# Kernel tuning notes

Hardware: AMD Instinct MI355X
Metric: run time of the kernel (lower is better)

The kernel has to match this reference:

```python
import jax, jax.numpy as jnp
import numpy as np

B, T, C, K, V = 4, 4096, 128, 64, 64
EPS = 1e-5


def layer_norm(x, g, b):
    mu = jnp.mean(x, axis=-1, keepdims=True)
    var = jnp.var(x, axis=-1, keepdims=True)
    return (x - mu) * jax.lax.rsqrt(var + EPS) * g + b


def setup_inputs() -> dict:
    key = jax.random.key(0)
    ks = jax.random.split(key, 8)
    s = 1.0 / np.sqrt(C)
    return {
        "x": jax.random.normal(ks[0], (B, T, C), dtype=jnp.float32),
        "Wq": jax.random.uniform(ks[1], (C, K), jnp.float32, -s, s),
        "bq": jnp.zeros((K,), jnp.float32),
        "Wk": jax.random.uniform(ks[2], (C, K), jnp.float32, -s, s),
        "bk": jnp.zeros((K,), jnp.float32),
        "Wv": jax.random.uniform(ks[3], (C, V), jnp.float32, -s, s),
        "bv": jnp.zeros((V,), jnp.float32),
        "gq": jnp.ones((K,), jnp.float32), "bgq": jnp.zeros((K,), jnp.float32),
        "gk": jnp.ones((K,), jnp.float32), "bgk": jnp.zeros((K,), jnp.float32),
        "gv": jnp.ones((V,), jnp.float32), "bgv": jnp.zeros((V,), jnp.float32),
        "go": jnp.ones((V,), jnp.float32), "bgo": jnp.zeros((V,), jnp.float32),
    }


def reference(x, Wq, bq, Wk, bk, Wv, bv, gq, bgq, gk, bgk, gv, bgv, go, bgo):
    # projections: B x T x {K,K,V}
    q = layer_norm(x @ Wq + bq, gq, bgq)
    k = layer_norm(x @ Wk + bk, gk, bgk)
    v = layer_norm(x @ Wv + bv, gv, bgv)
    sqrt_k = jnp.asarray(np.sqrt(K), x.dtype)
    # full B x T x T causal score matrix (faithful to the original bmm+mask)
    logits = jnp.einsum("btk,bsk->bts", q, k) / sqrt_k
    t = jnp.arange(T)
    causal = t[:, None] >= t[None, :]  # lower-triangular incl. diagonal
    logits = jnp.where(causal[None], logits, -jnp.inf)
    probs = jax.nn.softmax(logits, axis=-1)
    read = jnp.einsum("bts,bsv->btv", probs, v)
    read = layer_norm(read, go, bgo)
    return jnp.concatenate([x, read], axis=2)  # B x T x (C+V)
```

## Files before the change

### kernel.cpp

```cpp
#include <hip/hip_runtime.h>

#define TT 4096

typedef unsigned short u16;
typedef unsigned int u32;

typedef short bf16x8 __attribute__((ext_vector_type(8)));
typedef float f32x4 __attribute__((ext_vector_type(4)));

union U8 {
  uint2 q[2];
  uint4 u4;
  bf16x8 v;
  short s[8];
  u32 w[4];
};

static __device__ __forceinline__ u16 f2bf(float f) {
  union { float f; u32 u; } cv;
  cv.f = f;
  u32 r = cv.u + 0x7FFFu + ((cv.u >> 16) & 1u);
  return (u16)(r >> 16);
}
static __device__ __forceinline__ u32 pk2(float a, float b) {
  return (u32)f2bf(a) | ((u32)f2bf(b) << 16);
}
static __device__ __forceinline__ float bf2f(u16 h) {
  union { u32 u; float f; } cv;
  cv.u = ((u32)h) << 16;
  return cv.f;
}
static __device__ __forceinline__ float exp2a(float x) {
  float r; asm("v_exp_f32 %0, %1" : "=v"(r) : "v"(x)); return r;
}
static __device__ __forceinline__ u32 cvtpk(float lo, float hi) {
  u32 r; asm("v_cvt_pk_bf16_f32 %0, %1, %2" : "=v"(r) : "v"(lo), "v"(hi)); return r;
}

__global__ __launch_bounds__(64)
void wpack(const float* __restrict__ Wq, const float* __restrict__ Wk,
           const float* __restrict__ Wv, u16* __restrict__ wf)
{
  const int g = blockIdx.x;
  const int p = g >> 4, s = (g >> 2) & 3, nt = g & 3;
  const int l = threadIdx.x, lg = l >> 4, l15 = l & 15;
  const float* W = (p == 0) ? Wq : (p == 1) ? Wk : Wv;
  const int n = l15 + 16 * nt;
  U8 o;
#pragma unroll
  for (int j = 0; j < 8; ++j) {
    int k = 32 * s + ((j < 4) ? (4 * lg + j) : (16 + 4 * lg + (j - 4)));
    o.s[j] = (short)f2bf(W[k * 64 + n]);
  }
  *(uint4*)(wf + (size_t)(g * 64 + l) * 8) = o.u4;
}

__global__ __launch_bounds__(256)
void proj_mfma(const float* __restrict__ x, const u16* __restrict__ wf,
               const float* __restrict__ bq, const float* __restrict__ bk,
               const float* __restrict__ bv,
               const float* __restrict__ gq, const float* __restrict__ bgq,
               const float* __restrict__ gk, const float* __restrict__ bgk,
               const float* __restrict__ gv, const float* __restrict__ bgv,
               u16* __restrict__ qo, u16* __restrict__ ko, u16* __restrict__ vto,
               float* __restrict__ out)
{
  __shared__ u16 xs[64 * 128];
  const int bx = blockIdx.x;
  const int xcd = bx & 7, i = bx >> 3;
  const int tile = xcd * 32 + (i & 31);
  const int p = i >> 5;
  const int rowbase = tile * 64;
  const int t = threadIdx.x;

  {
    const int row = t >> 2, seg = t & 3;
    const float4* src = (const float4*)(x + (size_t)(rowbase + row) * 128 + seg * 32);
    float4 f[8];
#pragma unroll
    for (int q = 0; q < 8; ++q) f[q] = src[q];
    if ((p == 0 && seg < 2) || (p == 1 && seg >= 2)) {
      float4* dst = (float4*)(out + (size_t)(rowbase + row) * 192 + seg * 32);
#pragma unroll
      for (int q = 0; q < 8; ++q) dst[q] = f[q];
    }
    const int base = row * 256 + seg * 64;
    const int swz = (row & 7) << 4;
    char* xb = (char*)xs;
#pragma unroll
    for (int q = 0; q < 4; ++q) {
      uint4 u;
      u.x = pk2(f[2 * q].x, f[2 * q].y);
      u.y = pk2(f[2 * q].z, f[2 * q].w);
      u.z = pk2(f[2 * q + 1].x, f[2 * q + 1].y);
      u.w = pk2(f[2 * q + 1].z, f[2 * q + 1].w);
      *(uint4*)(xb + ((base + 16 * q) ^ swz)) = u;
    }
  }

  const int w = t >> 6, l = t & 63, lg = l >> 4, l15 = l & 15;
  U8 bfr[4][4];
  const u16* wp = wf + (size_t)p * (16 * 64 * 8);
#pragma unroll
  for (int s = 0; s < 4; ++s)
#pragma unroll
    for (int nt = 0; nt < 4; ++nt)
      bfr[s][nt].u4 = *(const uint4*)(wp + ((s * 4 + nt) * 64 + l) * 8);

  __syncthreads();

  f32x4 acc[4];
#pragma unroll
  for (int nt = 0; nt < 4; ++nt) acc[nt] = (f32x4){0.f, 0.f, 0.f, 0.f};
  const int abase = (16 * w + l15) * 256;
  const int aswz = (l15 & 7) << 4;
  const char* xb = (const char*)xs;
#pragma unroll
  for (int s = 0; s < 4; ++s) {
    U8 af;
    af.q[0] = *(const uint2*)(xb + ((abase + s * 64 + 8 * lg) ^ aswz));
    af.q[1] = *(const uint2*)(xb + ((abase + s * 64 + 8 * lg + 32) ^ aswz));
#pragma unroll
    for (int nt = 0; nt < 4; ++nt)
      acc[nt] = __builtin_amdgcn_mfma_f32_16x16x32_bf16(af.v, bfr[s][nt].v, acc[nt], 0, 0, 0);
  }

  const float* bb = (p == 0) ? bq : (p == 1) ? bk : bv;
  const float* gg = (p == 0) ? gq : (p == 1) ? gk : gv;
  const float* hh = (p == 0) ? bgq : (p == 1) ? bgk : bgv;
  float bcol[4], gcol[4], hcol[4];
#pragma unroll
  for (int nt = 0; nt < 4; ++nt) {
    int col = l15 + 16 * nt;
    bcol[nt] = bb[col]; gcol[nt] = gg[col]; hcol[nt] = hh[col];
  }
  float vals[4][4];
#pragma unroll
  for (int nt = 0; nt < 4; ++nt)
#pragma unroll
    for (int r = 0; r < 4; ++r) vals[nt][r] = acc[nt][r] + bcol[nt];

  float s1[4], s2[4];
#pragma unroll
  for (int r = 0; r < 4; ++r) {
    s1[r] = vals[0][r] + vals[1][r] + vals[2][r] + vals[3][r];
    s2[r] = vals[0][r] * vals[0][r] + vals[1][r] * vals[1][r]
          + vals[2][r] * vals[2][r] + vals[3][r] * vals[3][r];
#pragma unroll
    for (int d = 1; d < 16; d <<= 1) {
      s1[r] += __shfl_xor(s1[r], d);
      s2[r] += __shfl_xor(s2[r], d);
    }
  }

  if (p < 2) {
    u16* dst = (p == 0) ? qo : ko;
#pragma unroll
    for (int r = 0; r < 4; ++r) {
      float mu = s1[r] * (1.f / 64.f);
      float var = s2[r] * (1.f / 64.f) - mu * mu;
      float rs = rsqrtf(var + 1e-5f);
      int grow = rowbase + 16 * w + 4 * lg + r;
#pragma unroll
      for (int nt = 0; nt < 4; ++nt)
        dst[(size_t)grow * 64 + l15 + 16 * nt] =
            f2bf((vals[nt][r] - mu) * rs * gcol[nt] + hcol[nt]);
    }
  } else {
    const int b = rowbase >> 12;
    const int tl0 = (rowbase & 4095) + 16 * w + 4 * lg;
#pragma unroll
    for (int r = 0; r < 4; ++r) {
      float mu = s1[r] * (1.f / 64.f);
      float var = s2[r] * (1.f / 64.f) - mu * mu;
      float rs = rsqrtf(var + 1e-5f);
#pragma unroll
      for (int nt = 0; nt < 4; ++nt)
        vto[(size_t)(b * 64 + l15 + 16 * nt) * TT + tl0 + r] =
            f2bf((vals[nt][r] - mu) * rs * gcol[nt] + hcol[nt]);
    }
  }
}

__global__ __launch_bounds__(256)
void attn_seg4(const u16* __restrict__ qg, const u16* __restrict__ kg,
               const u16* __restrict__ vtg,
               float* __restrict__ mP, float* __restrict__ lP,
               u16* __restrict__ aP)
{
  __shared__ u16 kl4[4 * 64 * 64];
  __shared__ u16 vl4[4 * 64 * 64];
  const int bx = blockIdx.x;
  const int xcd = bx & 7, b = xcd >> 1, e = xcd & 1;
  const int j = e * 272 + (bx >> 3);
  int Q = 0;
  while (2 * (Q + 1) * (Q + 2) <= j) ++Q;
  const int ip = j - 2 * Q * (Q + 1);
  const int dv = ip / (Q + 1);
  const int q = 4 * Q + dv;
  const int s = ip - dv * (Q + 1);
  const int q0 = q * 64;
  const int it0 = s * 4;
  const int it1 = min(it0 + 4, q + 1);

  const int t = threadIdx.x;
  const int w = t >> 6, l = t & 63;
  const int l15 = l & 15, lg = l >> 4;
  const int swzl = (l15 & 7) << 4;

  const int qrow = q0 + 16 * w + l15;
  const u16* qrp = qg + (size_t)(b * TT + qrow) * 64;
  U8 qf[2];
#pragma unroll
  for (int hh = 0; hh < 2; ++hh) {
    qf[hh].q[0] = *(const uint2*)(qrp + 32 * hh + 4 * lg);
    qf[hh].q[1] = *(const uint2*)(qrp + 32 * hh + 4 * lg + 16);
  }

  {
    const int key = t >> 2, part = t & 3;
    const int sbase = key * 128 + part * 32;
    const int ssw = (key & 7) << 4;
    uint4 kr[4][2], vr[4][2];
#pragma unroll
    for (int tt = 0; tt < 4; ++tt) {
      int tile = it0 + tt; if (tile >= it1) tile = it1 - 1;
      const u16* ks = kg + (size_t)(b * TT + tile * 64 + key) * 64 + part * 16;
      kr[tt][0] = ((const uint4*)ks)[0];
      kr[tt][1] = ((const uint4*)ks)[1];
      const u16* vs = vtg + (size_t)(b * 64 + key) * TT + tile * 64 + part * 16;
      vr[tt][0] = ((const uint4*)vs)[0];
      vr[tt][1] = ((const uint4*)vs)[1];
    }
#pragma unroll
    for (int tt = 0; tt < 4; ++tt) {
      char* kd = (char*)kl4 + tt * 8192;
      char* vd = (char*)vl4 + tt * 8192;
      *(uint4*)(kd + ((sbase + 0) ^ ssw)) = kr[tt][0];
      *(uint4*)(kd + ((sbase + 16) ^ ssw)) = kr[tt][1];
      *(uint4*)(vd + ((sbase + 0) ^ ssw)) = vr[tt][0];
      *(uint4*)(vd + ((sbase + 16) ^ ssw)) = vr[tt][1];
    }
  }
  __syncthreads();

  const float C = 0.18033688011112042f;
  float m_run = -1e30f, l_run = 0.f;
  f32x4 acc[4];
#pragma unroll
  for (int ct = 0; ct < 4; ++ct) acc[ct] = (f32x4){0.f, 0.f, 0.f, 0.f};

  int toff = 0;
  for (int it = it0; it < it1; ++it, toff += 8192) {
    const int kb = it * 64;
    const char* kp = (const char*)kl4 + toff;
    const char* vp = (const char*)vl4 + toff;

    f32x4 st[4];
    __builtin_amdgcn_s_setprio(1);
#pragma unroll
    for (int t4 = 0; t4 < 4; ++t4) {
      const int rbase = (16 * t4 + l15) * 128 + 8 * lg;
      U8 kf0, kf1;
      kf0.q[0] = *(const uint2*)(kp + ((rbase + 0) ^ swzl));
      kf0.q[1] = *(const uint2*)(kp + ((rbase + 32) ^ swzl));
      kf1.q[0] = *(const uint2*)(kp + ((rbase + 64) ^ swzl));
      kf1.q[1] = *(const uint2*)(kp + ((rbase + 96) ^ swzl));
      f32x4 d = {0.f, 0.f, 0.f, 0.f};
      d = __builtin_amdgcn_mfma_f32_16x16x32_bf16(kf0.v, qf[0].v, d, 0, 0, 0);
      d = __builtin_amdgcn_mfma_f32_16x16x32_bf16(kf1.v, qf[1].v, d, 0, 0, 0);
      st[t4] = d;
    }
    __builtin_amdgcn_s_setprio(0);

    float sv[16];
    const bool needmask = (kb + 63 > q0 + 16 * w);
    if (needmask) {
#pragma unroll
      for (int t4 = 0; t4 < 4; ++t4) {
#pragma unroll
        for (int r = 0; r < 4; ++r) {
          float sc = st[t4][r] * C;
          int keyidx = kb + 16 * t4 + 4 * lg + r;
          sv[t4 * 4 + r] = (keyidx > qrow) ? -1e30f : sc;
        }
      }
    } else {
#pragma unroll
      for (int t4 = 0; t4 < 4; ++t4) {
#pragma unroll
        for (int r = 0; r < 4; ++r) sv[t4 * 4 + r] = st[t4][r] * C;
      }
    }
    float mx[8];
#pragma unroll
    for (int i = 0; i < 8; ++i) mx[i] = fmaxf(sv[2 * i], sv[2 * i + 1]);
#pragma unroll
    for (int i = 0; i < 4; ++i) mx[i] = fmaxf(mx[2 * i], mx[2 * i + 1]);
    float mt = fmaxf(fmaxf(mx[0], mx[1]), fmaxf(mx[2], mx[3]));
    mt = fmaxf(mt, __shfl_xor(mt, 16));
    mt = fmaxf(mt, __shfl_xor(mt, 32));

    if (!__all(mt - m_run <= 11.5f)) {
      const float mnew = fmaxf(m_run, mt);
      const float al = exp2a(m_run - mnew);
      l_run *= al;
      float ar[4];
#pragma unroll
      for (int r = 0; r < 4; ++r) ar[r] = __shfl(al, 4 * lg + r);
#pragma unroll
      for (int ct = 0; ct < 4; ++ct) {
#pragma unroll
        for (int r = 0; r < 4; ++r) acc[ct][r] *= ar[r];
      }
      m_run = mnew;
    }
    float p[16];
#pragma unroll
    for (int i = 0; i < 16; ++i) p[i] = exp2a(sv[i] - m_run);
    float sm[8];
#pragma unroll
    for (int i = 0; i < 8; ++i) sm[i] = p[2 * i] + p[2 * i + 1];
#pragma unroll
    for (int i = 0; i < 4; ++i) sm[i] = sm[2 * i] + sm[2 * i + 1];
    float rsum = (sm[0] + sm[1]) + (sm[2] + sm[3]);
    rsum += __shfl_xor(rsum, 16);
    rsum += __shfl_xor(rsum, 32);
    l_run += rsum;

    U8 pa[2];
#pragma unroll
    for (int u = 0; u < 2; ++u) {
#pragma unroll
      for (int k2 = 0; k2 < 4; ++k2)
        pa[u].w[k2] = cvtpk(p[8 * u + 2 * k2], p[8 * u + 2 * k2 + 1]);
    }

    __builtin_amdgcn_s_setprio(1);
#pragma unroll
    for (int ct = 0; ct < 4; ++ct) {
      const int vb = (16 * ct + l15) * 128 + 8 * lg;
#pragma unroll
      for (int u = 0; u < 2; ++u) {
        U8 vf;
        vf.q[0] = *(const uint2*)(vp + ((vb + 64 * u + 0) ^ swzl));
        vf.q[1] = *(const uint2*)(vp + ((vb + 64 * u + 32) ^ swzl));
        acc[ct] = __builtin_amdgcn_mfma_f32_16x16x32_bf16(pa[u].v, vf.v, acc[ct], 0, 0, 0);
      }
    }
    __builtin_amdgcn_s_setprio(0);
  }

  const size_t pbase = (size_t)(b * 544 + j) * 64;
  if (lg == 0) {
    mP[pbase + 16 * w + l15] = m_run;
    lP[pbase + 16 * w + l15] = l_run;
  }
#pragma unroll
  for (int ct = 0; ct < 4; ++ct) {
#pragma unroll
    for (int r = 0; r < 4; ++r) {
      int rin = 16 * w + 4 * lg + r;
      aP[(pbase + rin) * 64 + l15 + 16 * ct] = f2bf(acc[ct][r]);
    }
  }
}

__global__ __launch_bounds__(256)
void attn_merge4(const float* __restrict__ mP, const float* __restrict__ lP,
                 const u16* __restrict__ aP,
                 const float* __restrict__ go, const float* __restrict__ bgo,
                 float* __restrict__ out)
{
  const int t = threadIdx.x;
  const int w = t >> 6, c = t & 63;
  const int row = blockIdx.x * 4 + w;
  const int tid2 = row >> 6, rin = row & 63;
  const int b = tid2 >> 6, q = tid2 & 63;
  const int Q = q >> 2;
  const int base_q = b * 544 + 2 * Q * (Q + 1) + (q & 3) * (Q + 1);
  const int ns = Q + 1;

  float m = -1e30f, L = 0.f, o = 0.f;
  for (int s = 0; s < ns; ++s) {
    const size_t pb = (size_t)(base_q + s) * 64;
    float ms = mP[pb + rin];
    float ls = lP[pb + rin];
    float a = bf2f(aP[(pb + rin) * 64 + c]);
    float mn = fmaxf(m, ms);
    float w0 = exp2a(m - mn), w1 = exp2a(ms - mn);
    L = L * w0 + ls * w1;
    o = o * w0 + a * w1;
    m = mn;
  }
  o /= L;

  float s1 = o, s2 = o * o;
#pragma unroll
  for (int d = 1; d < 64; d <<= 1) {
    s1 += __shfl_xor(s1, d);
    s2 += __shfl_xor(s2, d);
  }
  float mu = s1 * (1.f / 64.f);
  float var = s2 * (1.f / 64.f) - mu * mu;
  float rs = rsqrtf(var + 1e-5f);
  out[(size_t)row * 192 + 128 + c] = (o - mu) * rs * go[c] + bgo[c];
}

__global__ __launch_bounds__(256)
void attn_splitW(const u16* __restrict__ qg, const u16* __restrict__ kg,
                 const u16* __restrict__ vtg,
                 float* __restrict__ mP, float* __restrict__ lP,
                 u16* __restrict__ aP,
                 int Wseg, int maxseg, int halfcnt)
{
  __shared__ u16 kl[64 * 64];
  __shared__ u16 vl[64 * 64];
  const int bx = blockIdx.x;
  const int xcd = bx & 7, b = xcd >> 1, e = xcd & 1;
  const int j = e * halfcnt + (bx >> 3);
  const int Wh = Wseg >> 1;
  int Q = 0;
  while (Wh * (Q + 1) * (Q + 2) <= j) ++Q;
  const int ip = j - Wh * Q * (Q + 1);
  const int dv = ip / (Q + 1);
  const int q = Wseg * Q + dv;
  const int s = ip - dv * (Q + 1);
  const int q0 = q * 64;
  const int tileid = b * 64 + q;
  const int it0 = s * Wseg;
  const int it1 = min(it0 + Wseg, q + 1);

  const int t = threadIdx.x;
  const int w = t >> 6, l = t & 63;
  const int l15 = l & 15, lg = l >> 4;
  const int swzl = (l15 & 7) << 4;

  const int qrow = q0 + 16 * w + l15;
  const u16* qrp = qg + (size_t)(b * TT + qrow) * 64;
  U8 qf[2];
#pragma unroll
  for (int hh = 0; hh < 2; ++hh) {
    qf[hh].q[0] = *(const uint2*)(qrp + 32 * hh + 4 * lg);
    qf[hh].q[1] = *(const uint2*)(qrp + 32 * hh + 4 * lg + 16);
  }

  const int key = t >> 2;
  const int part = t & 3;
  const int sbase = key * 128 + part * 32;
  const int ssw = (key & 7) << 4;
  uint4 kr0, kr1, vr0, vr1;
  {
    const u16* ks = kg + (size_t)(b * TT + it0 * 64 + key) * 64 + part * 16;
    kr0 = ((const uint4*)ks)[0];
    kr1 = ((const uint4*)ks)[1];
    const u16* vs = vtg + (size_t)(b * 64 + key) * TT + it0 * 64 + part * 16;
    vr0 = ((const uint4*)vs)[0];
    vr1 = ((const uint4*)vs)[1];
  }

  float m_run = -1e30f, l_run = 0.f;
  f32x4 acc[4];
#pragma unroll
  for (int ct = 0; ct < 4; ++ct) acc[ct] = (f32x4){0.f, 0.f, 0.f, 0.f};

  for (int it = it0; it < it1; ++it) {
    const int kb = it * 64;
    {
      char* kd = (char*)kl;
      char* vd = (char*)vl;
      *(uint4*)(kd + ((sbase + 0) ^ ssw)) = kr0;
      *(uint4*)(kd + ((sbase + 16) ^ ssw)) = kr1;
      *(uint4*)(vd + ((sbase + 0) ^ ssw)) = vr0;
      *(uint4*)(vd + ((sbase + 16) ^ ssw)) = vr1;
    }
    __syncthreads();
    if (it + 1 < it1) {
      const u16* ks = kg + (size_t)(b * TT + (it + 1) * 64 + key) * 64 + part * 16;
      kr0 = ((const uint4*)ks)[0];
      kr1 = ((const uint4*)ks)[1];
      const u16* vs = vtg + (size_t)(b * 64 + key) * TT + (it + 1) * 64 + part * 16;
      vr0 = ((const uint4*)vs)[0];
      vr1 = ((const uint4*)vs)[1];
    }

    f32x4 st[4];
#pragma unroll
    for (int t4 = 0; t4 < 4; ++t4) {
      const int rbase = (16 * t4 + l15) * 128 + 8 * lg;
      const char* kp = (const char*)kl;
      U8 kf0, kf1;
      kf0.q[0] = *(const uint2*)(kp + ((rbase + 0) ^ swzl));
      kf0.q[1] = *(const uint2*)(kp + ((rbase + 32) ^ swzl));
      kf1.q[0] = *(const uint2*)(kp + ((rbase + 64) ^ swzl));
      kf1.q[1] = *(const uint2*)(kp + ((rbase + 96) ^ swzl));
      f32x4 d = {0.f, 0.f, 0.f, 0.f};
      d = __builtin_amdgcn_mfma_f32_16x16x32_bf16(kf0.v, qf[0].v, d, 0, 0, 0);
      d = __builtin_amdgcn_mfma_f32_16x16x32_bf16(kf1.v, qf[1].v, d, 0, 0, 0);
      st[t4] = d;
    }

    float sv[16];
    const bool needmask = (kb + 63 > q0 + 16 * w);
#pragma unroll
    for (int t4 = 0; t4 < 4; ++t4) {
#pragma unroll
      for (int r = 0; r < 4; ++r) {
        float sc = st[t4][r] * 0.125f;
        if (needmask) {
          int keyidx = kb + 16 * t4 + 4 * lg + r;
          if (keyidx > qrow) sc = -1e30f;
        }
        sv[t4 * 4 + r] = sc;
      }
    }
    float mt = sv[0];
#pragma unroll
    for (int i = 1; i < 16; ++i) mt = fmaxf(mt, sv[i]);
    mt = fmaxf(mt, __shfl_xor(mt, 16));
    mt = fmaxf(mt, __shfl_xor(mt, 32));
    const float mnew = fmaxf(m_run, mt);
    const float al = __expf(m_run - mnew);
    float pv[16];
    float rsum = 0.f;
#pragma unroll
    for (int i = 0; i < 16; ++i) { pv[i] = __expf(sv[i] - mnew); rsum += pv[i]; }
    rsum += __shfl_xor(rsum, 16);
    rsum += __shfl_xor(rsum, 32);
    l_run = l_run * al + rsum;
    m_run = mnew;
    float ar[4];
#pragma unroll
    for (int r = 0; r < 4; ++r) ar[r] = __shfl(al, 4 * lg + r);
#pragma unroll
    for (int ct = 0; ct < 4; ++ct) {
#pragma unroll
      for (int r = 0; r < 4; ++r) acc[ct][r] *= ar[r];
    }
    U8 pa[2];
#pragma unroll
    for (int u = 0; u < 2; ++u) {
#pragma unroll
      for (int i = 0; i < 8; ++i) pa[u].s[i] = (short)f2bf(pv[8 * u + i]);
    }

#pragma unroll
    for (int ct = 0; ct < 4; ++ct) {
      const int vb = (16 * ct + l15) * 128 + 8 * lg;
      const char* vp = (const char*)vl;
#pragma unroll
      for (int u = 0; u < 2; ++u) {
        U8 vf;
        vf.q[0] = *(const uint2*)(vp + ((vb + 64 * u + 0) ^ swzl));
        vf.q[1] = *(const uint2*)(vp + ((vb + 64 * u + 32) ^ swzl));
        acc[ct] = __builtin_amdgcn_mfma_f32_16x16x32_bf16(pa[u].v, vf.v, acc[ct], 0, 0, 0);
      }
    }
    __syncthreads();
  }

  const size_t pbase = (size_t)(tileid * maxseg + s) * 64;
  if (lg == 0) {
    mP[pbase + 16 * w + l15] = m_run;
    lP[pbase + 16 * w + l15] = l_run;
  }
#pragma unroll
  for (int ct = 0; ct < 4; ++ct) {
#pragma unroll
    for (int r = 0; r < 4; ++r) {
      int rin = 16 * w + 4 * lg + r;
      aP[(pbase + rin) * 64 + l15 + 16 * ct] = f2bf(acc[ct][r]);
    }
  }
}

__global__ __launch_bounds__(256)
void attn_mergeW(const float* __restrict__ mP, const float* __restrict__ lP,
                 const u16* __restrict__ aP,
                 const float* __restrict__ go, const float* __restrict__ bgo,
                 float* __restrict__ out, int jshift, int maxseg)
{
  const int t = threadIdx.x;
  const int w = t >> 6, c = t & 63;
  const int row = blockIdx.x * 4 + w;
  const int tid2 = row >> 6, rin = row & 63;
  const int q = tid2 & 63;
  const int ns = (q >> jshift) + 1;

  float m = -1e30f, L = 0.f, o = 0.f;
  for (int s = 0; s < ns; ++s) {
    const size_t pbase = (size_t)(tid2 * maxseg + s) * 64;
    float ms = mP[pbase + rin];
    float ls = lP[pbase + rin];
    float a = bf2f(aP[(pbase + rin) * 64 + c]);
    float mn = fmaxf(m, ms);
    float w0 = __expf(m - mn), w1 = __expf(ms - mn);
    L = L * w0 + ls * w1;
    o = o * w0 + a * w1;
    m = mn;
  }
  o /= L;

  float s1 = o, s2 = o * o;
#pragma unroll
  for (int d = 1; d < 64; d <<= 1) {
    s1 += __shfl_xor(s1, d);
    s2 += __shfl_xor(s2, d);
  }
  float mu = s1 * (1.f / 64.f);
  float var = s2 * (1.f / 64.f) - mu * mu;
  float rs = rsqrtf(var + 1e-5f);
  out[(size_t)row * 192 + 128 + c] = (o - mu) * rs * go[c] + bgo[c];
}

__global__ __launch_bounds__(128)
void attn1(const u16* __restrict__ qg, const u16* __restrict__ kg,
           const u16* __restrict__ vtg,
           const float* __restrict__ go, const float* __restrict__ bgo,
           float* __restrict__ out)
{
  __shared__ u16 kl[64 * 64];
  __shared__ u16 vl[64 * 64];
  const int bx = blockIdx.x;
  const int tt = (bx < 256) ? bx : (767 - bx);
  const int b = tt >> 7;
  const int q0 = (tt & 127) * 32;
  const int tid = threadIdx.x;
  const int w = tid >> 6;
  const int l = tid & 63;
  const int l15 = l & 15;
  const int lg = l >> 4;
  const int swzl = (l15 & 7) << 4;

  const int qrow = q0 + 16 * w + l15;
  const u16* qrp = qg + (size_t)(b * TT + qrow) * 64;
  U8 qf[2];
#pragma unroll
  for (int h = 0; h < 2; ++h) {
    qf[h].q[0] = *(const uint2*)(qrp + 32 * h + 4 * lg);
    qf[h].q[1] = *(const uint2*)(qrp + 32 * h + 4 * lg + 16);
  }

  float m_run = -1e30f, l_run = 0.f;
  f32x4 acc[4];
#pragma unroll
  for (int ct = 0; ct < 4; ++ct) acc[ct] = (f32x4){0.f, 0.f, 0.f, 0.f};

  const int nkv = (q0 >> 6) + 1;
  for (int it = 0; it < nkv; ++it) {
    const int kb = it * 64;
    {
      const int key = tid >> 1;
      const int dh = (tid & 1) * 32;
      const u16* ks = kg + (size_t)(b * TT + kb + key) * 64 + dh;
      uint4 d0 = *(const uint4*)(ks + 0);
      uint4 d1 = *(const uint4*)(ks + 8);
      uint4 d2 = *(const uint4*)(ks + 16);
      uint4 d3 = *(const uint4*)(ks + 24);
      const int base = key * 128 + dh * 2;
      const int sw = (key & 7) << 4;
      char* kd = (char*)kl;
      *(uint4*)(kd + ((base + 0) ^ sw)) = d0;
      *(uint4*)(kd + ((base + 16) ^ sw)) = d1;
      *(uint4*)(kd + ((base + 32) ^ sw)) = d2;
      *(uint4*)(kd + ((base + 48) ^ sw)) = d3;
      const u16* vs = vtg + (size_t)(b * 64 + key) * TT + kb + dh;
      uint4 e0 = *(const uint4*)(vs + 0);
      uint4 e1 = *(const uint4*)(vs + 8);
      uint4 e2 = *(const uint4*)(vs + 16);
      uint4 e3 = *(const uint4*)(vs + 24);
      char* vd = (char*)vl;
      *(uint4*)(vd + ((base + 0) ^ sw)) = e0;
      *(uint4*)(vd + ((base + 16) ^ sw)) = e1;
      *(uint4*)(vd + ((base + 32) ^ sw)) = e2;
      *(uint4*)(vd + ((base + 48) ^ sw)) = e3;
    }
    __syncthreads();

    f32x4 st[4];
// ... 64 lines not shown
      for (int u = 0; u < 2; ++u) {
        U8 vf;
        vf.q[0] = *(const uint2*)(vp + ((vb + 64 * u + 0) ^ swzl));
        vf.q[1] = *(const uint2*)(vp + ((vb + 64 * u + 32) ^ swzl));
        acc[ct] = __builtin_amdgcn_mfma_f32_16x16x32_bf16(pa[u].v, vf.v, acc[ct], 0, 0, 0);
      }
    }
    __syncthreads();
  }

  float linv[4];
#pragma unroll
  for (int r = 0; r < 4; ++r) linv[r] = 1.f / __shfl(l_run, 4 * lg + r);
  float o[4][4];
#pragma unroll
  for (int ct = 0; ct < 4; ++ct) {
#pragma unroll
    for (int r = 0; r < 4; ++r) o[ct][r] = acc[ct][r] * linv[r];
  }
  float s1[4], s2[4];
#pragma unroll
  for (int r = 0; r < 4; ++r) {
    s1[r] = o[0][r] + o[1][r] + o[2][r] + o[3][r];
    s2[r] = o[0][r] * o[0][r] + o[1][r] * o[1][r] + o[2][r] * o[2][r] + o[3][r] * o[3][r];
#pragma unroll
    for (int d = 1; d < 16; d <<= 1) {
      s1[r] += __shfl_xor(s1[r], d);
      s2[r] += __shfl_xor(s2[r], d);
    }
  }
  float gov[4], bgv2[4];
#pragma unroll
  for (int ct = 0; ct < 4; ++ct) {
    gov[ct] = go[16 * ct + l15];
    bgv2[ct] = bgo[16 * ct + l15];
  }
#pragma unroll
  for (int r = 0; r < 4; ++r) {
    float mu = s1[r] * (1.f / 64.f);
    float var = s2[r] * (1.f / 64.f) - mu * mu;
    float rs = rsqrtf(var + 1e-5f);
    int row = q0 + 16 * w + 4 * lg + r;
    float* op = out + (size_t)(b * TT + row) * 192 + 128;
#pragma unroll
    for (int ct = 0; ct < 4; ++ct)
      op[16 * ct + l15] = (o[ct][r] - mu) * rs * gov[ct] + bgv2[ct];
  }
}

extern "C" void kernel_launch(void* const* d_in, const int* in_sizes, int n_in,
                              void* d_out, int out_size, void* d_ws, size_t ws_size,
                              hipStream_t stream) {
  (void)in_sizes; (void)n_in; (void)out_size;
  const float* x   = (const float*)d_in[0];
  const float* Wq  = (const float*)d_in[1];
  const float* bq  = (const float*)d_in[2];
  const float* Wk  = (const float*)d_in[3];
  const float* bk  = (const float*)d_in[4];
  const float* Wv  = (const float*)d_in[5];
  const float* bv  = (const float*)d_in[6];
  const float* gq  = (const float*)d_in[7];
  const float* bgq = (const float*)d_in[8];
  const float* gk  = (const float*)d_in[9];
  const float* bgk = (const float*)d_in[10];
  const float* gv  = (const float*)d_in[11];
  const float* bgv = (const float*)d_in[12];
  const float* go  = (const float*)d_in[13];
  const float* bgo = (const float*)d_in[14];
  float* out = (float*)d_out;

  char* wsb = (char*)d_ws;
  u16* qws  = (u16*)wsb;
  u16* kws  = (u16*)(wsb + (2u << 20));
  u16* vtws = (u16*)(wsb + (4u << 20));
  u16* wfr  = (u16*)(wsb + (6u << 20));
  const size_t OFF_MP = (6u << 20) + 65536;

  wpack<<<48, 64, 0, stream>>>(Wq, Wk, Wv, wfr);
  proj_mfma<<<768, 256, 0, stream>>>(x, wfr, bq, bk, bv,
                                     gq, bgq, gk, bgk, gv, bgv,
                                     qws, kws, vtws, out);

  {
    const size_t SEG4 = 4u * 544;
    const size_t MPS4 = SEG4 * 64 * 4;
    const size_t APS4 = SEG4 * 64 * 64 * 2;
    const size_t OFF_LP4 = OFF_MP + MPS4;
    const size_t OFF_AP4 = OFF_LP4 + MPS4;
    const size_t NEED4 = OFF_AP4 + APS4;
    const size_t MPS8 = 256u * 8 * 64 * 4;
    const size_t APS8 = 256u * 8 * 64 * 64 * 2;
    const size_t OFF_LP8 = OFF_MP + MPS8;
    const size_t OFF_AP8 = OFF_LP8 + MPS8;
    const size_t NEED8 = OFF_AP8 + APS8;
    const size_t MPS32 = 256u * 2 * 64 * 4;
    const size_t APS32 = 256u * 2 * 64 * 64 * 2;
    const size_t OFF_LP32 = OFF_MP + MPS32;
    const size_t OFF_AP32 = OFF_LP32 + MPS32;
    const size_t NEED32 = OFF_AP32 + APS32;

    if (ws_size >= NEED4) {
      float* mP = (float*)(wsb + OFF_MP);
      float* lP = (float*)(wsb + OFF_LP4);
      u16*   aP = (u16*)(wsb + OFF_AP4);
      attn_seg4<<<2176, 256, 0, stream>>>(qws, kws, vtws, mP, lP, aP);
      attn_merge4<<<4096, 256, 0, stream>>>(mP, lP, aP, go, bgo, out);
    } else if (ws_size >= NEED8) {
      float* mP = (float*)(wsb + OFF_MP);
      float* lP = (float*)(wsb + OFF_LP8);
      u16*   aP = (u16*)(wsb + OFF_AP8);
      attn_splitW<<<1152, 256, 0, stream>>>(qws, kws, vtws, mP, lP, aP, 8, 8, 144);
      attn_mergeW<<<4096, 256, 0, stream>>>(mP, lP, aP, go, bgo, out, 3, 8);
    } else if (ws_size >= NEED32) {
      float* mP = (float*)(wsb + OFF_MP);
      float* lP = (float*)(wsb + OFF_LP32);
      u16*   aP = (u16*)(wsb + OFF_AP32);
      attn_splitW<<<384, 256, 0, stream>>>(qws, kws, vtws, mP, lP, aP, 32, 2, 48);
      attn_mergeW<<<4096, 256, 0, stream>>>(mP, lP, aP, go, bgo, out, 5, 2);
    } else {
      attn1<<<512, 128, 0, stream>>>(qws, kws, vtws, go, bgo, out);
    }
  }
}
```

Before: 65.21 us.

## Split attention into two-tile segments and transpose V through LDS

Adds attn_seg2/attn_merge2, which split each query tile's causal key range into segments of two key tiles instead of four. This doubles the block count for more parallelism and smaller per-block LDS, with launch bounds asking for higher occupancy. The cost is more partial results to write and merge. Separately, the V projection output is now transposed through a padded shared-memory tile so each thread writes 16-byte vectors, replacing scattered 2-byte strided stores. Shared softmax code is moved into a helper, and the older splitW fallback paths are removed.

```diff
diff --git a/kernel.cpp b/kernel.cpp
--- a/kernel.cpp
+++ b/kernel.cpp
@@ -35,6 +35,73 @@
 }
 static __device__ __forceinline__ u32 cvtpk(float lo, float hi) {
   u32 r; asm("v_cvt_pk_bf16_f32 %0, %1, %2" : "=v"(r) : "v"(lo), "v"(hi)); return r;
+}
+
+static __device__ __forceinline__ void sm_step(
+    const f32x4* st, int kb, int wbase, int qrow, int lg,
+    float& m_run, float& l_run, f32x4* acc, U8* pa)
+{
+  const float C = 0.18033688011112042f;
+  float sv[16];
+  const bool needmask = (kb + 63 > wbase);
+  if (needmask) {
+#pragma unroll
+    for (int t4 = 0; t4 < 4; ++t4) {
+#pragma unroll
+      for (int r = 0; r < 4; ++r) {
+        float sc = st[t4][r] * C;
+        int keyidx = kb + 16 * t4 + 4 * lg + r;
+        sv[t4 * 4 + r] = (keyidx > qrow) ? -1e30f : sc;
+      }
+    }
+  } else {
+#pragma unroll
+    for (int t4 = 0; t4 < 4; ++t4) {
+#pragma unroll
+      for (int r = 0; r < 4; ++r) sv[t4 * 4 + r] = st[t4][r] * C;
+    }
+  }
+  float mx[8];
+#pragma unroll
+  for (int i = 0; i < 8; ++i) mx[i] = fmaxf(sv[2 * i], sv[2 * i + 1]);
+#pragma unroll
+  for (int i = 0; i < 4; ++i) mx[i] = fmaxf(mx[2 * i], mx[2 * i + 1]);
+  float mt = fmaxf(fmaxf(mx[0], mx[1]), fmaxf(mx[2], mx[3]));
+  mt = fmaxf(mt, __shfl_xor(mt, 16));
+  mt = fmaxf(mt, __shfl_xor(mt, 32));
+
+  if (!__all(mt - m_run <= 11.5f)) {
+    const float mnew = fmaxf(m_run, mt);
+    const float al = exp2a(m_run - mnew);
+    l_run *= al;
+    float ar[4];
+#pragma unroll
+    for (int r = 0; r < 4; ++r) ar[r] = __shfl(al, 4 * lg + r);
+#pragma unroll
+    for (int ct = 0; ct < 4; ++ct) {
+#pragma unroll
+      for (int r = 0; r < 4; ++r) acc[ct][r] *= ar[r];
+    }
+    m_run = mnew;
+  }
+  float p[16];
+#pragma unroll
+  for (int i = 0; i < 16; ++i) p[i] = exp2a(sv[i] - m_run);
+  float sm[8];
+#pragma unroll
+  for (int i = 0; i < 8; ++i) sm[i] = p[2 * i] + p[2 * i + 1];
+#pragma unroll
+  for (int i = 0; i < 4; ++i) sm[i] = sm[2 * i] + sm[2 * i + 1];
+  float rsum = (sm[0] + sm[1]) + (sm[2] + sm[3]);
+  rsum += __shfl_xor(rsum, 16);
+  rsum += __shfl_xor(rsum, 32);
+  l_run += rsum;
+#pragma unroll
+  for (int u = 0; u < 2; ++u) {
+#pragma unroll
+    for (int k2 = 0; k2 < 4; ++k2)
+      pa[u].w[k2] = cvtpk(p[8 * u + 2 * k2], p[8 * u + 2 * k2 + 1]);
+  }
 }
 
 __global__ __launch_bounds__(64)
@@ -65,7 +132,7 @@
                u16* __restrict__ qo, u16* __restrict__ ko, u16* __restrict__ vto,
                float* __restrict__ out)
 {
-  __shared__ u16 xs[64 * 128];
+  __shared__ u16 xs[64 * 130];
   const int bx = blockIdx.x;
   const int xcd = bx & 7, i = bx >> 3;
   const int tile = xcd * 32 + (i & 31);
@@ -167,48 +234,63 @@
             f2bf((vals[nt][r] - mu) * rs * gcol[nt] + hcol[nt]);
     }
   } else {
-    const int b = rowbase >> 12;
-    const int tl0 = (rowbase & 4095) + 16 * w + 4 * lg;
+    u16* vls = xs;
+    __syncthreads();
 #pragma unroll
     for (int r = 0; r < 4; ++r) {
       float mu = s1[r] * (1.f / 64.f);
       float var = s2[r] * (1.f / 64.f) - mu * mu;
       float rs = rsqrtf(var + 1e-5f);
+      int row = 16 * w + 4 * lg + r;
 #pragma unroll
       for (int nt = 0; nt < 4; ++nt)
-        vto[(size_t)(b * 64 + l15 + 16 * nt) * TT + tl0 + r] =
+        vls[row * 65 + l15 + 16 * nt] =
             f2bf((vals[nt][r] - mu) * rs * gcol[nt] + hcol[nt]);
     }
-  }
-}
-
-__global__ __launch_bounds__(256)
-void attn_seg4(const u16* __restrict__ qg, const u16* __restrict__ kg,
+    __syncthreads();
+    const int b = rowbase >> 12;
+    const int tl = rowbase & 4095;
+    const int col = t >> 2;
+    const int tq = (t & 3) * 16;
+    U8 o0, o1;
+#pragma unroll
+    for (int i = 0; i < 8; ++i) o0.s[i] = (short)vls[(tq + i) * 65 + col];
+#pragma unroll
+    for (int i = 0; i < 8; ++i) o1.s[i] = (short)vls[(tq + 8 + i) * 65 + col];
+    u16* dst = vto + (size_t)(b * 64 + col) * TT + tl + tq;
+    *(uint4*)(dst + 0) = o0.u4;
+    *(uint4*)(dst + 8) = o1.u4;
+  }
+}
+
+__global__ __launch_bounds__(256, 4)
+void attn_seg2(const u16* __restrict__ qg, const u16* __restrict__ kg,
                const u16* __restrict__ vtg,
                float* __restrict__ mP, float* __restrict__ lP,
                u16* __restrict__ aP)
 {
-  __shared__ u16 kl4[4 * 64 * 64];
-  __shared__ u16 vl4[4 * 64 * 64];
+  __shared__ u16 kl2[2 * 64 * 64];
+  __shared__ u16 vl2[2 * 64 * 64];
   const int bx = blockIdx.x;
-  const int xcd = bx & 7, b = xcd >> 1, e = xcd & 1;
-  const int j = e * 272 + (bx >> 3);
-  int Q = 0;
-  while (2 * (Q + 1) * (Q + 2) <= j) ++Q;
-  const int ip = j - 2 * Q * (Q + 1);
-  const int dv = ip / (Q + 1);
-  const int q = 4 * Q + dv;
-  const int s = ip - dv * (Q + 1);
+  const int xcd = bx & 7, b = xcd >> 1, e2 = xcd & 1;
+  const int j = e2 * 528 + (bx >> 3);
+  int G = 0;
+  while ((G + 1) * (G + 2) <= j) ++G;
+  const int ip = j - G * (G + 1);
+  const int e = (ip >= G + 1) ? 1 : 0;
+  const int s = ip - e * (G + 1);
+  const int q = 2 * G + e;
   const int q0 = q * 64;
-  const int it0 = s * 4;
-  const int it1 = min(it0 + 4, q + 1);
+  const int it0 = 2 * s;
+  const int it1 = min(it0 + 2, q + 1);
 
   const int t = threadIdx.x;
   const int w = t >> 6, l = t & 63;
   const int l15 = l & 15, lg = l >> 4;
   const int swzl = (l15 & 7) << 4;
 
-  const int qrow = q0 + 16 * w + l15;
+  const int wbase = q0 + 16 * w;
+  const int qrow = wbase + l15;
   const u16* qrp = qg + (size_t)(b * TT + qrow) * 64;
   U8 qf[2];
 #pragma unroll
@@ -221,9 +303,9 @@
     const int key = t >> 2, part = t & 3;
     const int sbase = key * 128 + part * 32;
     const int ssw = (key & 7) << 4;
-    uint4 kr[4][2], vr[4][2];
-#pragma unroll
-    for (int tt = 0; tt < 4; ++tt) {
+    uint4 kr[2][2], vr[2][2];
+#pragma unroll
+    for (int tt = 0; tt < 2; ++tt) {
       int tile = it0 + tt; if (tile >= it1) tile = it1 - 1;
       const u16* ks = kg + (size_t)(b * TT + tile * 64 + key) * 64 + part * 16;
       kr[tt][0] = ((const uint4*)ks)[0];
@@ -233,9 +315,9 @@
       vr[tt][1] = ((const uint4*)vs)[1];
     }
 #pragma unroll
-    for (int tt = 0; tt < 4; ++tt) {
-      char* kd = (char*)kl4 + tt * 8192;
-      char* vd = (char*)vl4 + tt * 8192;
+    for (int tt = 0; tt < 2; ++tt) {
+      char* kd = (char*)kl2 + tt * 8192;
+      char* vd = (char*)vl2 + tt * 8192;
       *(uint4*)(kd + ((sbase + 0) ^ ssw)) = kr[tt][0];
       *(uint4*)(kd + ((sbase + 16) ^ ssw)) = kr[tt][1];
       *(uint4*)(vd + ((sbase + 0) ^ ssw)) = vr[tt][0];
@@ -244,7 +326,6 @@
   }
   __syncthreads();
 
-  const float C = 0.18033688011112042f;
   float m_run = -1e30f, l_run = 0.f;
   f32x4 acc[4];
 #pragma unroll
@@ -253,8 +334,8 @@
   int toff = 0;
   for (int it = it0; it < it1; ++it, toff += 8192) {
     const int kb = it * 64;
-    const char* kp = (const char*)kl4 + toff;
-    const char* vp = (const char*)vl4 + toff;
+    const char* kp = (const char*)kl2 + toff;
+    const char* vp = (const char*)vl2 + toff;
 
     f32x4 st[4];
     __builtin_amdgcn_s_setprio(1);
@@ -273,68 +354,173 @@
     }
     __builtin_amdgcn_s_setprio(0);
 
-    float sv[16];
-    const bool needmask = (kb + 63 > q0 + 16 * w);
-    if (needmask) {
-#pragma unroll
-      for (int t4 = 0; t4 < 4; ++t4) {
-#pragma unroll
-        for (int r = 0; r < 4; ++r) {
-          float sc = st[t4][r] * C;
-          int keyidx = kb + 16 * t4 + 4 * lg + r;
-          sv[t4 * 4 + r] = (keyidx > qrow) ? -1e30f : sc;
-        }
+    U8 pa[2];
+    sm_step(st, kb, wbase, qrow, lg, m_run, l_run, acc, pa);
+
+    __builtin_amdgcn_s_setprio(1);
+#pragma unroll
+    for (int ct = 0; ct < 4; ++ct) {
+      const int vb = (16 * ct + l15) * 128 + 8 * lg;
+#pragma unroll
+      for (int u = 0; u < 2; ++u) {
+        U8 vf;
+        vf.q[0] = *(const uint2*)(vp + ((vb + 64 * u + 0) ^ swzl));
+        vf.q[1] = *(const uint2*)(vp + ((vb + 64 * u + 32) ^ swzl));
+        acc[ct] = __builtin_amdgcn_mfma_f32_16x16x32_bf16(pa[u].v, vf.v, acc[ct], 0, 0, 0);
       }
-    } else {
-#pragma unroll
-      for (int t4 = 0; t4 < 4; ++t4) {
-#pragma unroll
-        for (int r = 0; r < 4; ++r) sv[t4 * 4 + r] = st[t4][r] * C;
-      }
-    }
-    float mx[8];
-#pragma unroll
-    for (int i = 0; i < 8; ++i) mx[i] = fmaxf(sv[2 * i], sv[2 * i + 1]);
-#pragma unroll
-    for (int i = 0; i < 4; ++i) mx[i] = fmaxf(mx[2 * i], mx[2 * i + 1]);
-    float mt = fmaxf(fmaxf(mx[0], mx[1]), fmaxf(mx[2], mx[3]));
-    mt = fmaxf(mt, __shfl_xor(mt, 16));
-    mt = fmaxf(mt, __shfl_xor(mt, 32));
-
-    if (!__all(mt - m_run <= 11.5f)) {
-      const float mnew = fmaxf(m_run, mt);
-      const float al = exp2a(m_run - mnew);
-      l_run *= al;
-      float ar[4];
-#pragma unroll
-      for (int r = 0; r < 4; ++r) ar[r] = __shfl(al, 4 * lg + r);
-#pragma unroll
-      for (int ct = 0; ct < 4; ++ct) {
-#pragma unroll
-        for (int r = 0; r < 4; ++r) acc[ct][r] *= ar[r];
-      }
-      m_run = mnew;
-    }
-    float p[16];
-#pragma unroll
-    for (int i = 0; i < 16; ++i) p[i] = exp2a(sv[i] - m_run);
-    float sm[8];
-#pragma unroll
-    for (int i = 0; i < 8; ++i) sm[i] = p[2 * i] + p[2 * i + 1];
-#pragma unroll
-    for (int i = 0; i < 4; ++i) sm[i] = sm[2 * i] + sm[2 * i + 1];
-    float rsum = (sm[0] + sm[1]) + (sm[2] + sm[3]);
-    rsum += __shfl_xor(rsum, 16);
-    rsum += __shfl_xor(rsum, 32);
-    l_run += rsum;
+    }
+    __builtin_amdgcn_s_setprio(0);
+  }
+
+  const size_t pbase = (size_t)(b * 1056 + j) * 64;
+  if (lg == 0) {
+    mP[pbase + 16 * w + l15] = m_run;
+    lP[pbase + 16 * w + l15] = l_run;
+  }
+#pragma unroll
+  for (int ct = 0; ct < 4; ++ct) {
+#pragma unroll
+    for (int r = 0; r < 4; ++r) {
+      int rin = 16 * w + 4 * lg + r;
+      aP[(pbase + rin) * 64 + l15 + 16 * ct] = f2bf(acc[ct][r]);
+    }
+  }
+}
+
+__global__ __launch_bounds__(256)
+void attn_merge2(const float* __restrict__ mP, const float* __restrict__ lP,
+                 const u16* __restrict__ aP,
+                 const float* __restrict__ go, const float* __restrict__ bgo,
+                 float* __restrict__ out)
+{
+  const int t = threadIdx.x;
+  const int w = t >> 6, c = t & 63;
+  const int row = blockIdx.x * 4 + w;
+  const int tid2 = row >> 6, rin = row & 63;
+  const int b = tid2 >> 6, q = tid2 & 63;
+  const int Q = q >> 1;
+  const int base_q = b * 1056 + Q * (Q + 1) + (q & 1) * (Q + 1);
+  const int ns = Q + 1;
+
+  float m = -1e30f, L = 0.f, o = 0.f;
+  for (int s = 0; s < ns; ++s) {
+    const size_t pb = (size_t)(base_q + s) * 64;
+    float ms = mP[pb + rin];
+    float ls = lP[pb + rin];
+    float a = bf2f(aP[(pb + rin) * 64 + c]);
+    float mn = fmaxf(m, ms);
+    float w0 = exp2a(m - mn), w1 = exp2a(ms - mn);
+    L = L * w0 + ls * w1;
+    o = o * w0 + a * w1;
+    m = mn;
+  }
+  o /= L;
+
+  float s1 = o, s2 = o * o;
+#pragma unroll
+  for (int d = 1; d < 64; d <<= 1) {
+    s1 += __shfl_xor(s1, d);
+    s2 += __shfl_xor(s2, d);
+  }
+  float mu = s1 * (1.f / 64.f);
+  float var = s2 * (1.f / 64.f) - mu * mu;
+  float rs = rsqrtf(var + 1e-5f);
+  out[(size_t)row * 192 + 128 + c] = (o - mu) * rs * go[c] + bgo[c];
+}
+
+__global__ __launch_bounds__(256)
+void attn_seg4(const u16* __restrict__ qg, const u16* __restrict__ kg,
+               const u16* __restrict__ vtg,
+               float* __restrict__ mP, float* __restrict__ lP,
+               u16* __restrict__ aP)
+{
+  __shared__ u16 kl4[4 * 64 * 64];
+  __shared__ u16 vl4[4 * 64 * 64];
+  const int bx = blockIdx.x;
+  const int xcd = bx & 7, b = xcd >> 1, e2 = xcd & 1;
+  const int j = e2 * 272 + (bx >> 3);
+  int Q = 0;
+  while (2 * (Q + 1) * (Q + 2) <= j) ++Q;
+  const int ip = j - 2 * Q * (Q + 1);
+  const int dv = ip / (Q + 1);
+  const int q = 4 * Q + dv;
+  const int s = ip - dv * (Q + 1);
+  const int q0 = q * 64;
+  const int it0 = s * 4;
+  const int it1 = min(it0 + 4, q + 1);
+
+  const int t = threadIdx.x;
+  const int w = t >> 6, l = t & 63;
+  const int l15 = l & 15, lg = l >> 4;
+  const int swzl = (l15 & 7) << 4;
+
+  const int wbase = q0 + 16 * w;
+  const int qrow = wbase + l15;
+  const u16* qrp = qg + (size_t)(b * TT + qrow) * 64;
+  U8 qf[2];
+#pragma unroll
+  for (int hh = 0; hh < 2; ++hh) {
+    qf[hh].q[0] = *(const uint2*)(qrp + 32 * hh + 4 * lg);
+    qf[hh].q[1] = *(const uint2*)(qrp + 32 * hh + 4 * lg + 16);
+  }
+
+  {
+    const int key = t >> 2, part = t & 3;
+    const int sbase = key * 128 + part * 32;
+    const int ssw = (key & 7) << 4;
+    uint4 kr[4][2], vr[4][2];
+#pragma unroll
+    for (int tt = 0; tt < 4; ++tt) {
+      int tile = it0 + tt; if (tile >= it1) tile = it1 - 1;
+      const u16* ks = kg + (size_t)(b * TT + tile * 64 + key) * 64 + part * 16;
+      kr[tt][0] = ((const uint4*)ks)[0];
+      kr[tt][1] = ((const uint4*)ks)[1];
+      const u16* vs = vtg + (size_t)(b * 64 + key) * TT + tile * 64 + part * 16;
+      vr[tt][0] = ((const uint4*)vs)[0];
+      vr[tt][1] = ((const uint4*)vs)[1];
+    }
+#pragma unroll
+    for (int tt = 0; tt < 4; ++tt) {
+      char* kd = (char*)kl4 + tt * 8192;
+      char* vd = (char*)vl4 + tt * 8192;
+      *(uint4*)(kd + ((sbase + 0) ^ ssw)) = kr[tt][0];
+      *(uint4*)(kd + ((sbase + 16) ^ ssw)) = kr[tt][1];
+      *(uint4*)(vd + ((sbase + 0) ^ ssw)) = vr[tt][0];
+      *(uint4*)(vd + ((sbase + 16) ^ ssw)) = vr[tt][1];
+    }
+  }
+  __syncthreads();
+
+  float m_run = -1e30f, l_run = 0.f;
+  f32x4 acc[4];
+#pragma unroll
+  for (int ct = 0; ct < 4; ++ct) acc[ct] = (f32x4){0.f, 0.f, 0.f, 0.f};
+
+  int toff = 0;
+  for (int it = it0; it < it1; ++it, toff += 8192) {
+    const int kb = it * 64;
+    const char* kp = (const char*)kl4 + toff;
+    const char* vp = (const char*)vl4 + toff;
+
+    f32x4 st[4];
+    __builtin_amdgcn_s_setprio(1);
+#pragma unroll
+    for (int t4 = 0; t4 < 4; ++t4) {
+      const int rbase = (16 * t4 + l15) * 128 + 8 * lg;
+      U8 kf0, kf1;
+      kf0.q[0] = *(const uint2*)(kp + ((rbase + 0) ^ swzl));
+      kf0.q[1] = *(const uint2*)(kp + ((rbase + 32) ^ swzl));
+      kf1.q[0] = *(const uint2*)(kp + ((rbase + 64) ^ swzl));
+      kf1.q[1] = *(const uint2*)(kp + ((rbase + 96) ^ swzl));
+      f32x4 d = {0.f, 0.f, 0.f, 0.f};
+      d = __builtin_amdgcn_mfma_f32_16x16x32_bf16(kf0.v, qf[0].v, d, 0, 0, 0);
+      d = __builtin_amdgcn_mfma_f32_16x16x32_bf16(kf1.v, qf[1].v, d, 0, 0, 0);
+      st[t4] = d;
+    }
+    __builtin_amdgcn_s_setprio(0);
 
     U8 pa[2];
-#pragma unroll
-    for (int u = 0; u < 2; ++u) {
-#pragma unroll
-      for (int k2 = 0; k2 < 4; ++k2)
-        pa[u].w[k2] = cvtpk(p[8 * u + 2 * k2], p[8 * u + 2 * k2 + 1]);
-    }
+    sm_step(st, kb, wbase, qrow, lg, m_run, l_run, acc, pa);
 
     __builtin_amdgcn_s_setprio(1);
 #pragma unroll
@@ -389,212 +575,6 @@
     float a = bf2f(aP[(pb + rin) * 64 + c]);
     float mn = fmaxf(m, ms);
     float w0 = exp2a(m - mn), w1 = exp2a(ms - mn);
-    L = L * w0 + ls * w1;
-    o = o * w0 + a * w1;
-    m = mn;
-  }
-  o /= L;
-
-  float s1 = o, s2 = o * o;
-#pragma unroll
-  for (int d = 1; d < 64; d <<= 1) {
-    s1 += __shfl_xor(s1, d);
-    s2 += __shfl_xor(s2, d);
-  }
-  float mu = s1 * (1.f / 64.f);
-  float var = s2 * (1.f / 64.f) - mu * mu;
-  float rs = rsqrtf(var + 1e-5f);
-  out[(size_t)row * 192 + 128 + c] = (o - mu) * rs * go[c] + bgo[c];
-}
-
-__global__ __launch_bounds__(256)
-void attn_splitW(const u16* __restrict__ qg, const u16* __restrict__ kg,
-                 const u16* __restrict__ vtg,
-                 float* __restrict__ mP, float* __restrict__ lP,
-                 u16* __restrict__ aP,
-                 int Wseg, int maxseg, int halfcnt)
-{
-  __shared__ u16 kl[64 * 64];
-  __shared__ u16 vl[64 * 64];
-  const int bx = blockIdx.x;
-  const int xcd = bx & 7, b = xcd >> 1, e = xcd & 1;
-  const int j = e * halfcnt + (bx >> 3);
-  const int Wh = Wseg >> 1;
-  int Q = 0;
-  while (Wh * (Q + 1) * (Q + 2) <= j) ++Q;
-  const int ip = j - Wh * Q * (Q + 1);
-  const int dv = ip / (Q + 1);
-  const int q = Wseg * Q + dv;
-  const int s = ip - dv * (Q + 1);
-  const int q0 = q * 64;
-  const int tileid = b * 64 + q;
-  const int it0 = s * Wseg;
-  const int it1 = min(it0 + Wseg, q + 1);
-
-  const int t = threadIdx.x;
-  const int w = t >> 6, l = t & 63;
-  const int l15 = l & 15, lg = l >> 4;
-  const int swzl = (l15 & 7) << 4;
-
-  const int qrow = q0 + 16 * w + l15;
-  const u16* qrp = qg + (size_t)(b * TT + qrow) * 64;
-  U8 qf[2];
-#pragma unroll
-  for (int hh = 0; hh < 2; ++hh) {
-    qf[hh].q[0] = *(const uint2*)(qrp + 32 * hh + 4 * lg);
-    qf[hh].q[1] = *(const uint2*)(qrp + 32 * hh + 4 * lg + 16);
-  }
-
-  const int key = t >> 2;
-  const int part = t & 3;
-  const int sbase = key * 128 + part * 32;
-  const int ssw = (key & 7) << 4;
-  uint4 kr0, kr1, vr0, vr1;
-  {
-    const u16* ks = kg + (size_t)(b * TT + it0 * 64 + key) * 64 + part * 16;
-    kr0 = ((const uint4*)ks)[0];
-    kr1 = ((const uint4*)ks)[1];
-    const u16* vs = vtg + (size_t)(b * 64 + key) * TT + it0 * 64 + part * 16;
-    vr0 = ((const uint4*)vs)[0];
-    vr1 = ((const uint4*)vs)[1];
-  }
-
-  float m_run = -1e30f, l_run = 0.f;
-  f32x4 acc[4];
-#pragma unroll
-  for (int ct = 0; ct < 4; ++ct) acc[ct] = (f32x4){0.f, 0.f, 0.f, 0.f};
-
-  for (int it = it0; it < it1; ++it) {
-    const int kb = it * 64;
-    {
-      char* kd = (char*)kl;
-      char* vd = (char*)vl;
-      *(uint4*)(kd + ((sbase + 0) ^ ssw)) = kr0;
-      *(uint4*)(kd + ((sbase + 16) ^ ssw)) = kr1;
-      *(uint4*)(vd + ((sbase + 0) ^ ssw)) = vr0;
-      *(uint4*)(vd + ((sbase + 16) ^ ssw)) = vr1;
-    }
-    __syncthreads();
-    if (it + 1 < it1) {
-      const u16* ks = kg + (size_t)(b * TT + (it + 1) * 64 + key) * 64 + part * 16;
-      kr0 = ((const uint4*)ks)[0];
-      kr1 = ((const uint4*)ks)[1];
-      const u16* vs = vtg + (size_t)(b * 64 + key) * TT + (it + 1) * 64 + part * 16;
-      vr0 = ((const uint4*)vs)[0];
-      vr1 = ((const uint4*)vs)[1];
-    }
-
-    f32x4 st[4];
-#pragma unroll
-    for (int t4 = 0; t4 < 4; ++t4) {
-      const int rbase = (16 * t4 + l15) * 128 + 8 * lg;
-      const char* kp = (const char*)kl;
-      U8 kf0, kf1;
-      kf0.q[0] = *(const uint2*)(kp + ((rbase + 0) ^ swzl));
-      kf0.q[1] = *(const uint2*)(kp + ((rbase + 32) ^ swzl));
-      kf1.q[0] = *(const uint2*)(kp + ((rbase + 64) ^ swzl));
-      kf1.q[1] = *(const uint2*)(kp + ((rbase + 96) ^ swzl));
-      f32x4 d = {0.f, 0.f, 0.f, 0.f};
-      d = __builtin_amdgcn_mfma_f32_16x16x32_bf16(kf0.v, qf[0].v, d, 0, 0, 0);
-      d = __builtin_amdgcn_mfma_f32_16x16x32_bf16(kf1.v, qf[1].v, d, 0, 0, 0);
-      st[t4] = d;
-    }
-
-    float sv[16];
-    const bool needmask = (kb + 63 > q0 + 16 * w);
-#pragma unroll
-    for (int t4 = 0; t4 < 4; ++t4) {
-#pragma unroll
-      for (int r = 0; r < 4; ++r) {
-        float sc = st[t4][r] * 0.125f;
-        if (needmask) {
-          int keyidx = kb + 16 * t4 + 4 * lg + r;
-          if (keyidx > qrow) sc = -1e30f;
-        }
-        sv[t4 * 4 + r] = sc;
-      }
-    }
-    float mt = sv[0];
-#pragma unroll
-    for (int i = 1; i < 16; ++i) mt = fmaxf(mt, sv[i]);
-    mt = fmaxf(mt, __shfl_xor(mt, 16));
-    mt = fmaxf(mt, __shfl_xor(mt, 32));
-    const float mnew = fmaxf(m_run, mt);
-    const float al = __expf(m_run - mnew);
-    float pv[16];
-    float rsum = 0.f;
-#pragma unroll
-    for (int i = 0; i < 16; ++i) { pv[i] = __expf(sv[i] - mnew); rsum += pv[i]; }
-    rsum += __shfl_xor(rsum, 16);
-    rsum += __shfl_xor(rsum, 32);
-    l_run = l_run * al + rsum;
-    m_run = mnew;
-    float ar[4];
-#pragma unroll
-    for (int r = 0; r < 4; ++r) ar[r] = __shfl(al, 4 * lg + r);
-#pragma unroll
-    for (int ct = 0; ct < 4; ++ct) {
-#pragma unroll
-      for (int r = 0; r < 4; ++r) acc[ct][r] *= ar[r];
-    }
-    U8 pa[2];
-#pragma unroll
-    for (int u = 0; u < 2; ++u) {
-#pragma unroll
-      for (int i = 0; i < 8; ++i) pa[u].s[i] = (short)f2bf(pv[8 * u + i]);
-    }
-
-#pragma unroll
-    for (int ct = 0; ct < 4; ++ct) {
-      const int vb = (16 * ct + l15) * 128 + 8 * lg;
-      const char* vp = (const char*)vl;
-#pragma unroll
-      for (int u = 0; u < 2; ++u) {
-        U8 vf;
-        vf.q[0] = *(const uint2*)(vp + ((vb + 64 * u + 0) ^ swzl));
-        vf.q[1] = *(const uint2*)(vp + ((vb + 64 * u + 32) ^ swzl));
-        acc[ct] = __builtin_amdgcn_mfma_f32_16x16x32_bf16(pa[u].v, vf.v, acc[ct], 0, 0, 0);
-      }
-    }
-    __syncthreads();
-  }
-
-  const size_t pbase = (size_t)(tileid * maxseg + s) * 64;
-  if (lg == 0) {
-    mP[pbase + 16 * w + l15] = m_run;
-    lP[pbase + 16 * w + l15] = l_run;
-  }
-#pragma unroll
-  for (int ct = 0; ct < 4; ++ct) {
-#pragma unroll
-    for (int r = 0; r < 4; ++r) {
-      int rin = 16 * w + 4 * lg + r;
-      aP[(pbase + rin) * 64 + l15 + 16 * ct] = f2bf(acc[ct][r]);
-    }
-  }
-}
-
-__global__ __launch_bounds__(256)
-void attn_mergeW(const float* __restrict__ mP, const float* __restrict__ lP,
-                 const u16* __restrict__ aP,
-                 const float* __restrict__ go, const float* __restrict__ bgo,
-                 float* __restrict__ out, int jshift, int maxseg)
-{
-  const int t = threadIdx.x;
-  const int w = t >> 6, c = t & 63;
-  const int row = blockIdx.x * 4 + w;
-  const int tid2 = row >> 6, rin = row & 63;
-  const int q = tid2 & 63;
-  const int ns = (q >> jshift) + 1;
-
-  float m = -1e30f, L = 0.f, o = 0.f;
-  for (int s = 0; s < ns; ++s) {
-    const size_t pbase = (size_t)(tid2 * maxseg + s) * 64;
-    float ms = mP[pbase + rin];
-    float ls = lP[pbase + rin];
-    float a = bf2f(aP[(pbase + rin) * 64 + c]);
-    float mn = fmaxf(m, ms);
-    float w0 = __expf(m - mn), w1 = __expf(ms - mn);
     L = L * w0 + ls * w1;
     o = o * w0 + a * w1;
     m = mn;
@@ -825,41 +805,31 @@
                                      qws, kws, vtws, out);
 
   {
+    const size_t SEG2 = 4u * 1056;
+    const size_t MPS2 = SEG2 * 64 * 4;
+    const size_t APS2 = SEG2 * 64 * 64 * 2;
+    const size_t OFF_LP2 = OFF_MP + MPS2;
+    const size_t OFF_AP2 = OFF_LP2 + MPS2;
+    const size_t NEED2 = OFF_AP2 + APS2;
     const size_t SEG4 = 4u * 544;
     const size_t MPS4 = SEG4 * 64 * 4;
     const size_t APS4 = SEG4 * 64 * 64 * 2;
     const size_t OFF_LP4 = OFF_MP + MPS4;
     const size_t OFF_AP4 = OFF_LP4 + MPS4;
     const size_t NEED4 = OFF_AP4 + APS4;
-    const size_t MPS8 = 256u * 8 * 64 * 4;
-    const size_t APS8 = 256u * 8 * 64 * 64 * 2;
-    const size_t OFF_LP8 = OFF_MP + MPS8;
-    const size_t OFF_AP8 = OFF_LP8 + MPS8;
-    const size_t NEED8 = OFF_AP8 + APS8;
-    const size_t MPS32 = 256u * 2 * 64 * 4;
-    const size_t APS32 = 256u * 2 * 64 * 64 * 2;
-    const size_t OFF_LP32 = OFF_MP + MPS32;
-    const size_t OFF_AP32 = OFF_LP32 + MPS32;
-    const size_t NEED32 = OFF_AP32 + APS32;
-
-    if (ws_size >= NEED4) {
+
+    if (ws_size >= NEED2) {
+      float* mP = (float*)(wsb + OFF_MP);
+      float* lP = (float*)(wsb + OFF_LP2);
+      u16*   aP = (u16*)(wsb + OFF_AP2);
+      attn_seg2<<<4224, 256, 0, stream>>>(qws, kws, vtws, mP, lP, aP);
+      attn_merge2<<<4096, 256, 0, stream>>>(mP, lP, aP, go, bgo, out);
+    } else if (ws_size >= NEED4) {
       float* mP = (float*)(wsb + OFF_MP);
       float* lP = (float*)(wsb + OFF_LP4);
       u16*   aP = (u16*)(wsb + OFF_AP4);
       attn_seg4<<<2176, 256, 0, stream>>>(qws, kws, vtws, mP, lP, aP);
       attn_merge4<<<4096, 256, 0, stream>>>(mP, lP, aP, go, bgo, out);
-    } else if (ws_size >= NEED8) {
-      float* mP = (float*)(wsb + OFF_MP);
-      float* lP = (float*)(wsb + OFF_LP8);
-      u16*   aP = (u16*)(wsb + OFF_AP8);
-      attn_splitW<<<1152, 256, 0, stream>>>(qws, kws, vtws, mP, lP, aP, 8, 8, 144);
-      attn_mergeW<<<4096, 256, 0, stream>>>(mP, lP, aP, go, bgo, out, 3, 8);
-    } else if (ws_size >= NEED32) {
-      float* mP = (float*)(wsb + OFF_MP);
-      float* lP = (float*)(wsb + OFF_LP32);
-      u16*   aP = (u16*)(wsb + OFF_AP32);
-      attn_splitW<<<384, 256, 0, stream>>>(qws, kws, vtws, mP, lP, aP, 32, 2, 48);
-      attn_mergeW<<<4096, 256, 0, stream>>>(mP, lP, aP, go, bgo, out, 5, 2);
     } else {
       attn1<<<512, 128, 0, stream>>>(qws, kws, vtws, go, bgo, out);
     }
```

Result: slower. 68.21 us (+4.6%).
